# Kernel tuning notes

Measured on AMD Instinct MI355X. Metric: run time of the kernel, lower is better.

## Reference

```python
import jax, jax.numpy as jnp
import numpy as np

B, N, D_IN, D_OUT, NHOP = 16, 1024, 128, 128, 3


def setup_inputs() -> dict:
    key = jax.random.key(0)
    ks = jax.random.split(key, 7)
    x = jax.random.normal(ks[0], (B, N, D_IN), dtype=jnp.float32)
    # sparse-ish binary adjacency (float, as in the torch model) with self loops
    adj = (jax.random.uniform(ks[1], (B, N, N)) < 0.05).astype(jnp.float32)
    adj = jnp.maximum(adj, jnp.eye(N, dtype=jnp.float32)[None])
    # learned params (torch nn.Linear default-ish init scale)
    s_in = 1.0 / np.sqrt(D_IN)
    s_out = 1.0 / np.sqrt(2 * D_OUT)
    W_w = jax.random.uniform(ks[2], (D_OUT, D_IN), minval=-s_in, maxval=s_in, dtype=jnp.float32)
    W_b = jax.random.uniform(ks[3], (D_OUT,), minval=-s_in, maxval=s_in, dtype=jnp.float32)
    A = jax.random.normal(ks[4], (D_OUT, D_OUT), dtype=jnp.float32) * 0.02  # nn.Parameter(zeros) would kill signal; use small init
    gate_w = jax.random.uniform(ks[5], (1, 2 * D_OUT), minval=-s_out, maxval=s_out, dtype=jnp.float32)
    gate_b = jax.random.uniform(ks[6], (1,), minval=-s_out, maxval=s_out, dtype=jnp.float32)
    return {"x": x, "adj": adj, "W_w": W_w, "W_b": W_b, "A": A,
            "gate_w": gate_w, "gate_b": gate_b}


def reference(x, adj, W_w, W_b, A, gate_w, gate_b):
    # h = W(x): [B,N,D_OUT]
    h = jnp.einsum('bnd,od->bno', x, W_w) + W_b
    # bilinear score e[b,j,k] = (h A)_j . h_k, symmetrized
    e = jnp.einsum('bjl,bkl->bjk', jnp.einsum('bjd,de->bje', h, A), h)
    e = e + jnp.swapaxes(e, 1, 2)
    # masked softmax over dim=1 (as in the torch code), then re-mask
    att = jnp.where(adj > 0, e, jnp.zeros((), dtype=e.dtype))
    att = jax.nn.softmax(att, axis=1)
    att = att * adj
    retval = h
    for _ in range(NHOP):
        az = jax.nn.relu(jnp.einsum('bij,bjk->bik', att, retval))
        gate_in = jnp.concatenate([h, az], axis=-1)            # [B,N,2*D_OUT]
        coeff = jax.nn.sigmoid(jnp.einsum('bnf,of->bno', gate_in, gate_w) + gate_b)  # [B,N,1]
        retval = coeff * h + (1.0 - coeff) * az
    return retval
```

## Files before the change

kernel.cpp:

```cpp
#include <hip/hip_runtime.h>
#include <math.h>

#define Bn 16
#define Nn 1024
#define Dn 128

typedef unsigned short ushort;
typedef unsigned long long u64;
typedef short short8 __attribute__((ext_vector_type(8)));
typedef float f32x4 __attribute__((ext_vector_type(4)));
typedef ushort us8 __attribute__((ext_vector_type(8)));
typedef ushort us4 __attribute__((ext_vector_type(4)));

__device__ __forceinline__ ushort f2bf(float f) {
    unsigned u = __float_as_uint(f);
    u += 0x7fff + ((u >> 16) & 1);
    return (ushort)(u >> 16);
}
__device__ __forceinline__ float bf2f(ushort s) {
    return __uint_as_float(((unsigned)s) << 16);
}

#if defined(__has_builtin)
#if __has_builtin(__builtin_amdgcn_global_load_lds)
#define HAVE_GLL 1
#endif
#endif
#ifndef HAVE_GLL
#define HAVE_GLL 0
#endif

typedef __attribute__((address_space(1))) void as1_t;
typedef __attribute__((address_space(3))) void as3_t;

__device__ __forceinline__ void stage_group(const void* gbase, void* lbase, int lane) {
#if HAVE_GLL
    __builtin_amdgcn_global_load_lds((as1_t*)((const char*)gbase + lane * 16),
                                     (as3_t*)lbase, 16, 0, 0);
#else
    *(us8*)((char*)lbase + lane * 16) = *(const us8*)((const char*)gbase + lane * 16);
#endif
}


__global__ __launch_bounds__(256) void k_ph0(const float* __restrict__ Ww,
                                             const float* __restrict__ A,
                                             const float* __restrict__ adj,
                                             ushort* __restrict__ Whi, ushort* __restrict__ Wlo,
                                             ushort* __restrict__ Shi, ushort* __restrict__ Slo,
                                             float* __restrict__ Z, u64* __restrict__ bm) {
    int L = blockIdx.x, t = threadIdx.x;
    if (L < 64) {
        int i = L * 256 + t;
        float w = Ww[i];
        ushort wh = f2bf(w);
        Whi[i] = wh;
        Wlo[i] = f2bf(w - bf2f(wh));
        int e = i >> 7, d = i & 127;
        float s = A[i] + A[d * Dn + e];
        ushort sh = f2bf(s);
        Shi[i] = sh;
        Slo[i] = f2bf(s - bf2f(sh));
        Z[i] = (float)Nn;
    }
    int gwv = L * 4 + (t >> 6);
    int lane = t & 63;
    #pragma unroll 4
    for (int it = 0; it < 16; ++it) {
        int pair = gwv * 16 + it;
        const float* p = adj + (size_t)pair * 256 + lane * 4;
        float4 v = *(const float4*)p;
        u64 b0 = __ballot(v.x > 0.f);
        u64 b1 = __ballot(v.y > 0.f);
        u64 b2 = __ballot(v.z > 0.f);
        u64 b3 = __ballot(v.w > 0.f);
        if (lane == 0) {
            u64* d = bm + (size_t)pair * 4;
            d[0] = b0; d[1] = b1; d[2] = b2; d[3] = b3;
        }
    }
}

__global__ __launch_bounds__(256) void k_h(const float* __restrict__ x,
                                           const float* __restrict__ Wb,
                                           const ushort* __restrict__ Whi,
                                           const ushort* __restrict__ Wlo,
                                           const ushort* __restrict__ Shi,
                                           const ushort* __restrict__ Slo,
                                           float* __restrict__ h,
                                           ushort* __restrict__ h16f,
                                           ushort* __restrict__ g16f) {
    int I0 = blockIdx.x * 16;
    int t = threadIdx.x, w = t >> 6, lane = t & 63;
    int m = lane & 15, q = lane >> 4;

    __shared__ float xs[16][Dn + 4];
    __shared__ float hs[16][Dn + 4];
    __shared__ float gs_[16][Dn + 4];

    {
        int r = t >> 4, c8 = (t & 15) * 8;
        const float* src = x + (size_t)(I0 + r) * Dn + c8;
        *(float4*)&xs[r][c8]     = *(const float4*)(src);
        *(float4*)&xs[r][c8 + 4] = *(const float4*)(src + 4);
    }
    __syncthreads();

    f32x4 acc0 = {0,0,0,0}, acc1 = {0,0,0,0};
    #pragma unroll
    for (int ks = 0; ks < 4; ++ks) {
        int k0 = q * 8 + ks * 32;
        float v[8]; short8 ahi, alo;
        *(float4*)(v)     = *(const float4*)(&xs[m][k0]);
        *(float4*)(v + 4) = *(const float4*)(&xs[m][k0 + 4]);
        #pragma unroll
        for (int j = 0; j < 8; ++j) {
            ushort hi = f2bf(v[j]);
            ahi[j] = (short)hi;
            alo[j] = (short)f2bf(v[j] - bf2f(hi));
        }
        #pragma unroll
        for (int nn = 0; nn < 2; ++nn) {
            int brow = (w * 2 + nn) * 16 + m;
            short8 bhi = __builtin_bit_cast(short8, ((const us8*)(Whi + (size_t)brow * Dn))[q + ks * 4]);
            short8 blo = __builtin_bit_cast(short8, ((const us8*)(Wlo + (size_t)brow * Dn))[q + ks * 4]);
            f32x4 acc = nn ? acc1 : acc0;
            acc = __builtin_amdgcn_mfma_f32_16x16x32_bf16(ahi, bhi, acc, 0, 0, 0);
            acc = __builtin_amdgcn_mfma_f32_16x16x32_bf16(alo, bhi, acc, 0, 0, 0);
            acc = __builtin_amdgcn_mfma_f32_16x16x32_bf16(ahi, blo, acc, 0, 0, 0);
            if (nn) acc1 = acc; else acc0 = acc;
        }
    }
    #pragma unroll
    for (int nn = 0; nn < 2; ++nn) {
        int col = (w * 2 + nn) * 16 + m;
        float bias = Wb[col];
        f32x4 acc = nn ? acc1 : acc0;
        #pragma unroll
        for (int r = 0; r < 4; ++r) {
            int rl = q * 4 + r;
            float hv = acc[r] + bias;
            h[(size_t)(I0 + rl) * Dn + col] = hv;
            hs[rl][col] = hv;
        }
    }
    __syncthreads();

    f32x4 bcc0 = {0,0,0,0}, bcc1 = {0,0,0,0};
    #pragma unroll
    for (int ks = 0; ks < 4; ++ks) {
        int k0 = q * 8 + ks * 32;
        float v[8]; short8 ahi, alo;
        *(float4*)(v)     = *(const float4*)(&hs[m][k0]);
        *(float4*)(v + 4) = *(const float4*)(&hs[m][k0 + 4]);
        #pragma unroll
        for (int j = 0; j < 8; ++j) {
            ushort hi = f2bf(v[j]);
            ahi[j] = (short)hi;
            alo[j] = (short)f2bf(v[j] - bf2f(hi));
        }
        #pragma unroll
        for (int nn = 0; nn < 2; ++nn) {
            int brow = (w * 2 + nn) * 16 + m;
            short8 bhi = __builtin_bit_cast(short8, ((const us8*)(Shi + (size_t)brow * Dn))[q + ks * 4]);
            short8 blo = __builtin_bit_cast(short8, ((const us8*)(Slo + (size_t)brow * Dn))[q + ks * 4]);
            f32x4 acc = nn ? bcc1 : bcc0;
            acc = __builtin_amdgcn_mfma_f32_16x16x32_bf16(ahi, bhi, acc, 0, 0, 0);
            acc = __builtin_amdgcn_mfma_f32_16x16x32_bf16(alo, bhi, acc, 0, 0, 0);
            acc = __builtin_amdgcn_mfma_f32_16x16x32_bf16(ahi, blo, acc, 0, 0, 0);
            if (nn) bcc1 = acc; else bcc0 = acc;
        }
    }
    #pragma unroll
    for (int nn = 0; nn < 2; ++nn) {
        int col = (w * 2 + nn) * 16 + m;
        f32x4 acc = nn ? bcc1 : bcc0;
        #pragma unroll
        for (int r = 0; r < 4; ++r)
            gs_[q * 4 + r][col] = acc[r];
    }
    __syncthreads();

    {
        int kc = t >> 6, mm = (t >> 2) & 15, qq = t & 3;
        int cb = kc * 32 + qq * 8;
        us8 oh, oa;
        #pragma unroll
        for (int e = 0; e < 8; ++e) {
            oh[e] = f2bf(hs[mm][cb + e]);
            oa[e] = f2bf(gs_[mm][cb + e]);
        }
        size_t U = (size_t)(I0 >> 4) * 256 + kc * 64 + qq * 16 + mm;
        ((us8*)h16f)[U] = oh;
        ((us8*)g16f)[U] = oa;
    }
}

__global__ __launch_bounds__(256, 4) void k_scores(const ushort* __restrict__ g16f,
                                                   const ushort* __restrict__ h16f,
                                                   const u64* __restrict__ bm,
                                                   ushort* __restrict__ Ef,
                                                   float* __restrict__ Z) {
    int L = blockIdx.x;
    int b    = ((L & 7) << 1) | (L >> 11);
    int tile = (L >> 3) & 255;
    int I0 = (tile >> 4) << 6;
    int J0 = (tile & 15) << 6;
    int t = threadIdx.x, wid = t >> 6, lane = t & 63;
    int loff = lane * 16;

    __shared__ __align__(16) char smem[18432];
    float (*sc)[68] = (float(*)[68])smem;
    float (*cz)[64] = (float(*)[64])(smem + 17408);

    {
        const char* hbp = (const char*)h16f + (size_t)b * 262144;
        for (int g = wid; g < 16; g += 4) {
            int rt_l = g >> 2, kk = g & 3;
            stage_group(hbp + ((size_t)((J0 >> 4) + rt_l) * 256 + kk * 64) * 16,
                        smem + g * 1024, lane);
        }
    }
    short8 afr[4];
    {
        const char* gbp = (const char*)g16f + (size_t)b * 262144
                        + (size_t)((I0 >> 4) + wid) * 4096 + loff;
        #pragma unroll
        for (int ks = 0; ks < 4; ++ks)
            afr[ks] = __builtin_bit_cast(short8, *(const us8*)(gbp + ks * 1024));
    }
    __syncthreads();

    f32x4 acc[4] = {};
    #pragma unroll
    for (int ks = 0; ks < 4; ++ks) {
        #pragma unroll
        for (int nt = 0; nt < 4; ++nt) {
            short8 bb = __builtin_bit_cast(short8,
                *(const us8*)(smem + (nt * 4 + ks) * 1024 + loff));
            acc[nt] = __builtin_amdgcn_mfma_f32_16x16x32_bf16(afr[ks], bb, acc[nt], 0, 0, 0);
        }
    }
    __syncthreads();

    {
        int m = lane & 15, q = lane >> 4;
        #pragma unroll
        for (int nt = 0; nt < 4; ++nt)
            #pragma unroll
            for (int r = 0; r < 4; ++r)
                sc[wid * 16 + q * 4 + r][nt * 16 + m] = acc[nt][r];
    }
    __syncthreads();

    int row16 = t >> 4, c = t & 15;
    int bitc = ((J0 >> 2) & 63) + c;
    float colsum[4] = {0.f, 0.f, 0.f, 0.f};
    #pragma unroll
    for (int it = 0; it < 4; ++it) {
        int row = it * 16 + row16;
        const u64* wp = bm + ((size_t)(b * Nn + I0 + row) * 4 + (J0 >> 8)) * 4;
        u64 wj[4] = {wp[0], wp[1], wp[2], wp[3]};
        float s4[4];
        *(float4*)s4 = *(const float4*)(&sc[row][c * 4]);
        us4 e4;
        #pragma unroll
        for (int j = 0; j < 4; ++j) {
            float ex = __expf(s4[j]);
            bool on = (wj[j] >> bitc) & 1;
            e4[j] = f2bf(on ? ex : 0.f);
            colsum[j] += on ? (ex - 1.0f) : 0.f;
        }
        size_t base = ((((size_t)b * 64 + (I0 >> 4) + it) * 32 + (J0 >> 5) + (c >> 3)) * 512)
                    + (size_t)((c & 7) >> 1) * 128 + row16 * 8 + (c & 1) * 4;
        *(us4*)(Ef + base) = e4;
    }
    #pragma unroll
    for (int j = 0; j < 4; ++j) {
        colsum[j] += __shfl_xor(colsum[j], 16, 64);
        colsum[j] += __shfl_xor(colsum[j], 32, 64);
    }
    if (lane < 16) {
        #pragma unroll
        for (int j = 0; j < 4; ++j) cz[wid][lane * 4 + j] = colsum[j];
    }
    __syncthreads();
    if (t < 64) {
        float s = cz[0][t] + cz[1][t] + cz[2][t] + cz[3][t];
        atomicAdd(&Z[b * Nn + J0 + t], s);
    }
}

__global__ __launch_bounds__(256) void k_prep(const float* __restrict__ src,
                                              const float* __restrict__ Z,
                                              ushort* __restrict__ Tf) {
    int b = blockIdx.y;
    int j0 = blockIdx.x * 64;
    int t = threadIdx.x;
    __shared__ float ls[64][129];
    __shared__ float iz[64];
    if (t < 64) iz[t] = 1.0f / Z[b * Nn + j0 + t];
    __syncthreads();
    #pragma unroll
    for (int it = 0; it < 8; ++it) {
        int idx = it * 256 + t;
        int j = idx >> 5, k4 = (idx & 31) * 4;
        float4 v = *(const float4*)(src + ((size_t)b * Nn + j0 + j) * Dn + k4);
        float z = iz[j];
        ls[j][k4] = v.x * z; ls[j][k4 + 1] = v.y * z;
        ls[j][k4 + 2] = v.z * z; ls[j][k4 + 3] = v.w * z;
    }
    __syncthreads();
    int k = t & 127, half = t >> 7;
    us8 o[4];
    #pragma unroll
    for (int qq = 0; qq < 4; ++qq) {
        us8 tmp;
        #pragma unroll
        for (int e = 0; e < 8; ++e)
            tmp[e] = f2bf(ls[half * 32 + qq * 8 + e][k]);
        o[qq] = tmp;
    }
    size_t G = (size_t)(k >> 4) * 32 + (j0 >> 5) + half;
    ushort* dst = Tf + (size_t)b * 131072 + G * 512 + (size_t)(k & 15) * 8;
    #pragma unroll
    for (int qq = 0; qq < 4; ++qq)
        *(us8*)(dst + qq * 128) = o[qq];
}

#define STAGEB(BUF, cch) do {                                                          \
    for (int g = w; g < 32; g += 8)                                                    \
        stage_group(tfb + ((size_t)(g >> 2) * 32 + (cch) * 4 + (g & 3)) * 1024,        \
                    smem + (BUF) * 32768 + g * 1024, lane);                            \
} while (0)

#define ELOAD(SET, cch) do {                                                           \
    _Pragma("unroll")                                                                  \
    for (int kk = 0; kk < 4; ++kk)                                                     \
        SET[kk] = __builtin_bit_cast(short8,                                           \
            *(const us8*)(ebase + ((cch) * 4 + kk) * 1024));                           \
} while (0)

#define MFMAC(BUF, SET) do {                                                           \
    _Pragma("unroll")                                                                  \
    for (int kk = 0; kk < 4; ++kk) {                                                   \
        _Pragma("unroll")                                                              \
        for (int nt2 = 0; nt2 < 4; ++nt2) {                                            \
            short8 bf = __builtin_bit_cast(short8,                                     \
                *(const us8*)(smem + (BUF) * 32768 + choff + (nt2 * 4 + kk) * 1024 + loff)); \
            acc[nt2] = __builtin_amdgcn_mfma_f32_16x16x32_bf16(SET[kk], bf, acc[nt2], 0, 0, 0); \
        }                                                                              \
    }                                                                                  \
} while (0)

#define WAITB(NC) do {                                                                 \
    asm volatile("s_waitcnt vmcnt(" #NC ")" ::: "memory");                             \
    __builtin_amdgcn_s_barrier();                                                      \
} while (0)

__global__ __launch_bounds__(512, 1) void k_hop(const ushort* __restrict__ Ef,
                                                const ushort* __restrict__ Tf,
                                                const float* __restrict__ h,
                                                const float* __restrict__ Z,
                                                const float* __restrict__ gw,
                                                const float* __restrict__ gb,
                                                ushort* __restrict__ Tfn,
                                                float* __restrict__ out,
                                                int last) {
    int L = blockIdx.x;
    int b  = ((L & 7) << 1) | (L >> 7);
    int t4 = (L >> 3) & 15;
    int t = threadIdx.x, w = t >> 6, lane = t & 63;
    int m = lane & 15, q = lane >> 4;
    int wr = w & 3, ch = w >> 2;
    int rt = t4 * 4 + wr;
    int I0 = rt << 4;
    int loff = lane * 16;
    int choff = ch * 16384;

    __shared__ __align__(16) char smem[98304];
    __shared__ float gpart[4][16][2];

    const char* tfb   = (const char*)Tf + (size_t)b * 262144;
    const char* ebase = (const char*)Ef + (size_t)(b * 64 + rt) * 32768 + loff;

    f32x4 acc[4] = {};
    short8 aA[4], aB[4], aC[4];

    STAGEB(0, 0); ELOAD(aA, 0);
    STAGEB(1, 1); ELOAD(aB, 1);

    WAITB(8); STAGEB(2, 2); ELOAD(aC, 2); MFMAC(0, aA);
    WAITB(8); STAGEB(0, 3); ELOAD(aA, 3); MFMAC(1, aB);
    WAITB(8); STAGEB(1, 4); ELOAD(aB, 4); MFMAC(2, aC);
    WAITB(8); STAGEB(2, 5); ELOAD(aC, 5); MFMAC(0, aA);
    WAITB(8); STAGEB(0, 6); ELOAD(aA, 6); MFMAC(1, aB);
    WAITB(8); STAGEB(1, 7); ELOAD(aB, 7); MFMAC(2, aC);
    WAITB(8);                             MFMAC(0, aA);
    WAITB(0);                             MFMAC(1, aB);

    float gb0 = gb[0];
    float gwa[4], gwz[4];
    #pragma unroll
    for (int nt2 = 0; nt2 < 4; ++nt2) {
        gwa[nt2] = gw[ch * 64 + nt2 * 16 + m];
        gwz[nt2] = gw[Dn + ch * 64 + nt2 * 16 + m];
    }

    float hv[4][4], gsr[4];
    size_t hbase = ((size_t)b * Nn + I0) * Dn;
    #pragma unroll
    for (int r = 0; r < 4; ++r) {
        int row = q * 4 + r;
        float gs = 0.f;
        #pragma unroll
        for (int nt2 = 0; nt2 < 4; ++nt2) {
            float az = fmaxf(acc[nt2][r], 0.f);
            acc[nt2][r] = az;
            float hh = h[hbase + (size_t)row * Dn + ch * 64 + nt2 * 16 + m];
            hv[nt2][r] = hh;
            gs += hh * gwa[nt2] + az * gwz[nt2];
        }
        gs += __shfl_xor(gs, 1, 64);
        gs += __shfl_xor(gs, 2, 64);
        gs += __shfl_xor(gs, 4, 64);
        gs += __shfl_xor(gs, 8, 64);
        gsr[r] = gs;
    }
    if (m == 0) {
        #pragma unroll
        for (int r = 0; r < 4; ++r) gpart[wr][q * 4 + r][ch] = gsr[r];
    }
    __syncthreads();

    float coef[4];
    #pragma unroll
    for (int r = 0; r < 4; ++r) {
        float g2 = gpart[wr][q * 4 + r][0] + gpart[wr][q * 4 + r][1];
        coef[r] = 1.0f / (1.0f + __expf(-(g2 + gb0)));
    }

    if (last) {
        #pragma unroll
        for (int r = 0; r < 4; ++r) {
            int row = q * 4 + r;
            float cc = coef[r];
            #pragma unroll
            for (int nt2 = 0; nt2 < 4; ++nt2)
                out[hbase + (size_t)row * Dn + ch * 64 + nt2 * 16 + m] =
                    cc * hv[nt2][r] + (1.f - cc) * acc[nt2][r];
        }
    } else {
        ushort (*tt)[128][16] = (ushort(*)[128][16])smem;
        #pragma unroll
        for (int r = 0; r < 4; ++r) {
            int row = q * 4 + r;
            float cc = coef[r];
            float iz = 1.0f / Z[b * Nn + I0 + row];
            #pragma unroll
            for (int nt2 = 0; nt2 < 4; ++nt2) {
                float v = cc * hv[nt2][r] + (1.f - cc) * acc[nt2][r];
                tt[wr][ch * 64 + nt2 * 16 + m][row] = f2bf(v * iz);
            }
        }
        __syncthreads();
        if (t < 256) {
            int k = t >> 1, jh = t & 1;
            size_t G = (size_t)(k >> 4) * 32 + t4 * 2 + jh;
            ushort* dst = Tfn + (size_t)b * 131072 + G * 512 + (size_t)(k & 15) * 8;
            #pragma unroll
            for (int qq = 0; qq < 4; ++qq)
                *(us8*)(dst + qq * 128) = *(const us8*)&tt[jh * 2 + (qq >> 1)][k][(qq & 1) * 8];
        }
    }
}

extern "C" void kernel_launch(void* const* d_in, const int* in_sizes, int n_in,
                              void* d_out, int out_size, void* d_ws, size_t ws_size,
                              hipStream_t stream) {
    const float* x    = (const float*)d_in[0];
    const float* adj  = (const float*)d_in[1];
    const float* Ww   = (const float*)d_in[2];
    const float* Wb   = (const float*)d_in[3];
    const float* A    = (const float*)d_in[4];
    const float* gw   = (const float*)d_in[5];
    const float* gb   = (const float*)d_in[6];
    float* out = (float*)d_out;

    char* ws = (char*)d_ws;
    float*  h    = (float*)(ws);
    ushort* Ta   = (ushort*)(ws + (8u << 20));
    ushort* Tb   = (ushort*)(ws + (12u << 20));
    ushort* E    = (ushort*)(ws + (16u << 20));
    float*  Z    = (float*)(ws + (48u << 20));
    ushort* Whi  = (ushort*)(ws + (48u << 20) + (64u << 10));
    ushort* Wlo  = (ushort*)(ws + (48u << 20) + (96u << 10));
    ushort* Shi  = (ushort*)(ws + (48u << 20) + (128u << 10));
    ushort* Slo  = (ushort*)(ws + (48u << 20) + (160u << 10));
    u64*    bm   = (u64*)(ws + (48u << 20) + (192u << 10));

    k_ph0   <<<1024, 256, 0, stream>>>(Ww, A, adj, Whi, Wlo, Shi, Slo, Z, bm);
    k_h     <<<1024, 256, 0, stream>>>(x, Wb, Whi, Wlo, Shi, Slo, h, Ta, Tb);
    k_scores<<<4096, 256, 0, stream>>>(Tb, Ta, bm, E, Z);
    k_prep  <<<dim3(16, Bn), 256, 0, stream>>>(h, Z, Ta);
    k_hop   <<<256, 512, 0, stream>>>(E, Ta, h, Z, gw, gb, Tb, out, 0);
    k_hop   <<<256, 512, 0, stream>>>(E, Tb, h, Z, gw, gb, Ta, out, 0);
    k_hop   <<<256, 512, 0, stream>>>(E, Ta, h, Z, gw, gb, (ushort*)nullptr, out, 1);
}
```

Baseline: 192.1 us.

## Fuse hop kernels into one persistent kernel with grid barriers; fold prep and bitmask

Replaces the prep kernel and the three separate hop launches with a single persistent kernel of 128 blocks. Each block handles two row tiles and uses an atomic-counter grid barrier between hops, and it keeps h and 1/Z in registers across hops. The adjacency bitmask build moves into k_h, and the k_scores epilogue is rewritten to write 8-wide E stores with shuffle-based column sums. This removes launch overhead and repeated h loads, but halves the grid size, which cuts parallelism per hop, and adds spin-barrier costs that assume all blocks are co-resident.

```diff
diff --git a/kernel.cpp b/kernel.cpp
--- a/kernel.cpp
+++ b/kernel.cpp
@@ -42,29 +42,158 @@
 #endif
 }
 
-
-__global__ __launch_bounds__(256) void k_ph0(const float* __restrict__ Ww,
-                                             const float* __restrict__ A,
-                                             const float* __restrict__ adj,
-                                             ushort* __restrict__ Whi, ushort* __restrict__ Wlo,
-                                             ushort* __restrict__ Shi, ushort* __restrict__ Slo,
-                                             float* __restrict__ Z, u64* __restrict__ bm) {
-    int L = blockIdx.x, t = threadIdx.x;
-    if (L < 64) {
-        int i = L * 256 + t;
-        float w = Ww[i];
-        ushort wh = f2bf(w);
-        Whi[i] = wh;
-        Wlo[i] = f2bf(w - bf2f(wh));
-        int e = i >> 7, d = i & 127;
-        float s = A[i] + A[d * Dn + e];
-        ushort sh = f2bf(s);
-        Shi[i] = sh;
-        Slo[i] = f2bf(s - bf2f(sh));
-        Z[i] = (float)Nn;
-    }
-    int gwv = L * 4 + (t >> 6);
-    int lane = t & 63;
+__device__ __forceinline__ void gbar(int* bar, int phase, int nblk) {
+    __syncthreads();
+    if (threadIdx.x == 0) {
+        __threadfence();
+        int old = atomicAdd(&bar[0], 1);
+        if (old == phase * nblk - 1)
+            __hip_atomic_store(&bar[1], phase, __ATOMIC_RELAXED, __HIP_MEMORY_SCOPE_AGENT);
+        while (__hip_atomic_load(&bar[1], __ATOMIC_RELAXED, __HIP_MEMORY_SCOPE_AGENT) < phase)
+            __builtin_amdgcn_s_sleep(2);
+        __threadfence();
+    }
+    __syncthreads();
+}
+
+
+__global__ __launch_bounds__(256) void k_W(const float* __restrict__ Ww,
+                                           const float* __restrict__ A,
+                                           ushort* __restrict__ Whi, ushort* __restrict__ Wlo,
+                                           ushort* __restrict__ Shi, ushort* __restrict__ Slo,
+                                           float* __restrict__ Z, int* __restrict__ bar) {
+    int i = blockIdx.x * 256 + threadIdx.x;
+    float w = Ww[i];
+    ushort wh = f2bf(w);
+    Whi[i] = wh;
+    Wlo[i] = f2bf(w - bf2f(wh));
+    int e = i >> 7, d = i & 127;
+    float s = A[i] + A[d * Dn + e];
+    ushort sh = f2bf(s);
+    Shi[i] = sh;
+    Slo[i] = f2bf(s - bf2f(sh));
+    Z[i] = (float)Nn;
+    if (i == 0) { bar[0] = 0; bar[1] = 0; }
+}
+
+__global__ __launch_bounds__(256) void k_h(const float* __restrict__ x,
+                                           const float* __restrict__ adj,
+                                           const float* __restrict__ Wb,
+                                           const ushort* __restrict__ Whi,
+                                           const ushort* __restrict__ Wlo,
+                                           const ushort* __restrict__ Shi,
+                                           const ushort* __restrict__ Slo,
+                                           float* __restrict__ h,
+                                           ushort* __restrict__ h16f,
+                                           ushort* __restrict__ g16f,
+                                           u64* __restrict__ bm) {
+    int L = blockIdx.x;
+    int I0 = L * 16;
+    int t = threadIdx.x, w = t >> 6, lane = t & 63;
+    int m = lane & 15, q = lane >> 4;
+
+    __shared__ float xs[16][Dn + 4];
+    __shared__ float hs[16][Dn + 4];
+    __shared__ float gs_[16][Dn + 4];
+
+    {
+        int r = t >> 4, c8 = (t & 15) * 8;
+        const float* src = x + (size_t)(I0 + r) * Dn + c8;
+        *(float4*)&xs[r][c8]     = *(const float4*)(src);
+        *(float4*)&xs[r][c8 + 4] = *(const float4*)(src + 4);
+    }
+    __syncthreads();
+
+    f32x4 acc0 = {0,0,0,0}, acc1 = {0,0,0,0};
+    #pragma unroll
+    for (int ks = 0; ks < 4; ++ks) {
+        int k0 = q * 8 + ks * 32;
+        float v[8]; short8 ahi, alo;
+        *(float4*)(v)     = *(const float4*)(&xs[m][k0]);
+        *(float4*)(v + 4) = *(const float4*)(&xs[m][k0 + 4]);
+        #pragma unroll
+        for (int j = 0; j < 8; ++j) {
+            ushort hi = f2bf(v[j]);
+            ahi[j] = (short)hi;
+            alo[j] = (short)f2bf(v[j] - bf2f(hi));
+        }
+        #pragma unroll
+        for (int nn = 0; nn < 2; ++nn) {
+            int brow = (w * 2 + nn) * 16 + m;
+            short8 bhi = __builtin_bit_cast(short8, ((const us8*)(Whi + (size_t)brow * Dn))[q + ks * 4]);
+            short8 blo = __builtin_bit_cast(short8, ((const us8*)(Wlo + (size_t)brow * Dn))[q + ks * 4]);
+            f32x4 acc = nn ? acc1 : acc0;
+            acc = __builtin_amdgcn_mfma_f32_16x16x32_bf16(ahi, bhi, acc, 0, 0, 0);
+            acc = __builtin_amdgcn_mfma_f32_16x16x32_bf16(alo, bhi, acc, 0, 0, 0);
+            acc = __builtin_amdgcn_mfma_f32_16x16x32_bf16(ahi, blo, acc, 0, 0, 0);
+            if (nn) acc1 = acc; else acc0 = acc;
+        }
+    }
+    #pragma unroll
+    for (int nn = 0; nn < 2; ++nn) {
+        int col = (w * 2 + nn) * 16 + m;
+        float bias = Wb[col];
+        f32x4 acc = nn ? acc1 : acc0;
+        #pragma unroll
+        for (int r = 0; r < 4; ++r) {
+            int rl = q * 4 + r;
+            float hv = acc[r] + bias;
+            h[(size_t)(I0 + rl) * Dn + col] = hv;
+            hs[rl][col] = hv;
+        }
+    }
+    __syncthreads();
+
+    f32x4 bcc0 = {0,0,0,0}, bcc1 = {0,0,0,0};
+    #pragma unroll
+    for (int ks = 0; ks < 4; ++ks) {
+        int k0 = q * 8 + ks * 32;
+        float v[8]; short8 ahi, alo;
+        *(float4*)(v)     = *(const float4*)(&hs[m][k0]);
+        *(float4*)(v + 4) = *(const float4*)(&hs[m][k0 + 4]);
+        #pragma unroll
+        for (int j = 0; j < 8; ++j) {
+            ushort hi = f2bf(v[j]);
+            ahi[j] = (short)hi;
+            alo[j] = (short)f2bf(v[j] - bf2f(hi));
+        }
+        #pragma unroll
+        for (int nn = 0; nn < 2; ++nn) {
+            int brow = (w * 2 + nn) * 16 + m;
+            short8 bhi = __builtin_bit_cast(short8, ((const us8*)(Shi + (size_t)brow * Dn))[q + ks * 4]);
+            short8 blo = __builtin_bit_cast(short8, ((const us8*)(Slo + (size_t)brow * Dn))[q + ks * 4]);
+            f32x4 acc = nn ? bcc1 : bcc0;
+            acc = __builtin_amdgcn_mfma_f32_16x16x32_bf16(ahi, bhi, acc, 0, 0, 0);
+            acc = __builtin_amdgcn_mfma_f32_16x16x32_bf16(alo, bhi, acc, 0, 0, 0);
+            acc = __builtin_amdgcn_mfma_f32_16x16x32_bf16(ahi, blo, acc, 0, 0, 0);
+            if (nn) bcc1 = acc; else bcc0 = acc;
+        }
+    }
+    #pragma unroll
+    for (int nn = 0; nn < 2; ++nn) {
+        int col = (w * 2 + nn) * 16 + m;
+        f32x4 acc = nn ? bcc1 : bcc0;
+        #pragma unroll
+        for (int r = 0; r < 4; ++r)
+            gs_[q * 4 + r][col] = acc[r];
+    }
+    __syncthreads();
+
+    {
+        int kc = t >> 6, mm = (t >> 2) & 15, qq = t & 3;
+        int cb = kc * 32 + qq * 8;
+        us8 oh, oa;
+        #pragma unroll
+        for (int e = 0; e < 8; ++e) {
+            oh[e] = f2bf(hs[mm][cb + e]);
+            oa[e] = f2bf(gs_[mm][cb + e]);
+        }
+        size_t U = (size_t)L * 256 + kc * 64 + qq * 16 + mm;
+        ((us8*)h16f)[U] = oh;
+        ((us8*)g16f)[U] = oa;
+    }
+
+    int gwv = L * 4 + w;
     #pragma unroll 4
     for (int it = 0; it < 16; ++it) {
         int pair = gwv * 16 + it;
@@ -81,121 +210,6 @@
     }
 }
 
-__global__ __launch_bounds__(256) void k_h(const float* __restrict__ x,
-                                           const float* __restrict__ Wb,
-                                           const ushort* __restrict__ Whi,
-                                           const ushort* __restrict__ Wlo,
-                                           const ushort* __restrict__ Shi,
-                                           const ushort* __restrict__ Slo,
-                                           float* __restrict__ h,
-                                           ushort* __restrict__ h16f,
-                                           ushort* __restrict__ g16f) {
-    int I0 = blockIdx.x * 16;
-    int t = threadIdx.x, w = t >> 6, lane = t & 63;
-    int m = lane & 15, q = lane >> 4;
-
-    __shared__ float xs[16][Dn + 4];
-    __shared__ float hs[16][Dn + 4];
-    __shared__ float gs_[16][Dn + 4];
-
-    {
-        int r = t >> 4, c8 = (t & 15) * 8;
-        const float* src = x + (size_t)(I0 + r) * Dn + c8;
-        *(float4*)&xs[r][c8]     = *(const float4*)(src);
-        *(float4*)&xs[r][c8 + 4] = *(const float4*)(src + 4);
-    }
-    __syncthreads();
-
-    f32x4 acc0 = {0,0,0,0}, acc1 = {0,0,0,0};
-    #pragma unroll
-    for (int ks = 0; ks < 4; ++ks) {
-        int k0 = q * 8 + ks * 32;
-        float v[8]; short8 ahi, alo;
-        *(float4*)(v)     = *(const float4*)(&xs[m][k0]);
-        *(float4*)(v + 4) = *(const float4*)(&xs[m][k0 + 4]);
-        #pragma unroll
-        for (int j = 0; j < 8; ++j) {
-            ushort hi = f2bf(v[j]);
-            ahi[j] = (short)hi;
-            alo[j] = (short)f2bf(v[j] - bf2f(hi));
-        }
-        #pragma unroll
-        for (int nn = 0; nn < 2; ++nn) {
-            int brow = (w * 2 + nn) * 16 + m;
-            short8 bhi = __builtin_bit_cast(short8, ((const us8*)(Whi + (size_t)brow * Dn))[q + ks * 4]);
-            short8 blo = __builtin_bit_cast(short8, ((const us8*)(Wlo + (size_t)brow * Dn))[q + ks * 4]);
-            f32x4 acc = nn ? acc1 : acc0;
-            acc = __builtin_amdgcn_mfma_f32_16x16x32_bf16(ahi, bhi, acc, 0, 0, 0);
-            acc = __builtin_amdgcn_mfma_f32_16x16x32_bf16(alo, bhi, acc, 0, 0, 0);
-            acc = __builtin_amdgcn_mfma_f32_16x16x32_bf16(ahi, blo, acc, 0, 0, 0);
-            if (nn) acc1 = acc; else acc0 = acc;
-        }
-    }
-    #pragma unroll
-    for (int nn = 0; nn < 2; ++nn) {
-        int col = (w * 2 + nn) * 16 + m;
-        float bias = Wb[col];
-        f32x4 acc = nn ? acc1 : acc0;
-        #pragma unroll
-        for (int r = 0; r < 4; ++r) {
-            int rl = q * 4 + r;
-            float hv = acc[r] + bias;
-            h[(size_t)(I0 + rl) * Dn + col] = hv;
-            hs[rl][col] = hv;
-        }
-    }
-    __syncthreads();
-
-    f32x4 bcc0 = {0,0,0,0}, bcc1 = {0,0,0,0};
-    #pragma unroll
-    for (int ks = 0; ks < 4; ++ks) {
-        int k0 = q * 8 + ks * 32;
-        float v[8]; short8 ahi, alo;
-        *(float4*)(v)     = *(const float4*)(&hs[m][k0]);
-        *(float4*)(v + 4) = *(const float4*)(&hs[m][k0 + 4]);
-        #pragma unroll
-        for (int j = 0; j < 8; ++j) {
-            ushort hi = f2bf(v[j]);
-            ahi[j] = (short)hi;
-            alo[j] = (short)f2bf(v[j] - bf2f(hi));
-        }
-        #pragma unroll
-        for (int nn = 0; nn < 2; ++nn) {
-            int brow = (w * 2 + nn) * 16 + m;
-            short8 bhi = __builtin_bit_cast(short8, ((const us8*)(Shi + (size_t)brow * Dn))[q + ks * 4]);
-            short8 blo = __builtin_bit_cast(short8, ((const us8*)(Slo + (size_t)brow * Dn))[q + ks * 4]);
-            f32x4 acc = nn ? bcc1 : bcc0;
-            acc = __builtin_amdgcn_mfma_f32_16x16x32_bf16(ahi, bhi, acc, 0, 0, 0);
-            acc = __builtin_amdgcn_mfma_f32_16x16x32_bf16(alo, bhi, acc, 0, 0, 0);
-            acc = __builtin_amdgcn_mfma_f32_16x16x32_bf16(ahi, blo, acc, 0, 0, 0);
-            if (nn) bcc1 = acc; else bcc0 = acc;
-        }
-    }
-    #pragma unroll
-    for (int nn = 0; nn < 2; ++nn) {
-        int col = (w * 2 + nn) * 16 + m;
-        f32x4 acc = nn ? bcc1 : bcc0;
-        #pragma unroll
-        for (int r = 0; r < 4; ++r)
-            gs_[q * 4 + r][col] = acc[r];
-    }
-    __syncthreads();
-
-    {
-        int kc = t >> 6, mm = (t >> 2) & 15, qq = t & 3;
-        int cb = kc * 32 + qq * 8;
-        us8 oh, oa;
-        #pragma unroll
-        for (int e = 0; e < 8; ++e) {
-            oh[e] = f2bf(hs[mm][cb + e]);
-            oa[e] = f2bf(gs_[mm][cb + e]);
-        }
-        size_t U = (size_t)(I0 >> 4) * 256 + kc * 64 + qq * 16 + mm;
-        ((us8*)h16f)[U] = oh;
-        ((us8*)g16f)[U] = oa;
-    }
-}
-
 __global__ __launch_bounds__(256, 4) void k_scores(const ushort* __restrict__ g16f,
                                                    const ushort* __restrict__ h16f,
                                                    const u64* __restrict__ bm,
@@ -211,7 +225,7 @@
 
     __shared__ __align__(16) char smem[18432];
     float (*sc)[68] = (float(*)[68])smem;
-    float (*cz)[64] = (float(*)[64])(smem + 17408);
+    float (*cz8)[32] = (float(*)[32])(smem + 17408);
 
     {
         const char* hbp = (const char*)h16f + (size_t)b * 262144;
@@ -253,79 +267,44 @@
     }
     __syncthreads();
 
-    int row16 = t >> 4, c = t & 15;
-    int bitc = ((J0 >> 2) & 63) + c;
-    float colsum[4] = {0.f, 0.f, 0.f, 0.f};
-    #pragma unroll
-    for (int it = 0; it < 4; ++it) {
-        int row = it * 16 + row16;
+    int mm = lane & 15, qq = lane >> 4;
+    #pragma unroll
+    for (int rep = 0; rep < 2; ++rep) {
+        int gidx = wid + rep * 4;
+        int it = gidx >> 1, kcg = gidx & 1;
+        int row = it * 16 + mm;
+        int c0 = kcg * 32 + qq * 8;
         const u64* wp = bm + ((size_t)(b * Nn + I0 + row) * 4 + (J0 >> 8)) * 4;
         u64 wj[4] = {wp[0], wp[1], wp[2], wp[3]};
-        float s4[4];
-        *(float4*)s4 = *(const float4*)(&sc[row][c * 4]);
-        us4 e4;
-        #pragma unroll
-        for (int j = 0; j < 4; ++j) {
-            float ex = __expf(s4[j]);
-            bool on = (wj[j] >> bitc) & 1;
-            e4[j] = f2bf(on ? ex : 0.f);
-            colsum[j] += on ? (ex - 1.0f) : 0.f;
-        }
-        size_t base = ((((size_t)b * 64 + (I0 >> 4) + it) * 32 + (J0 >> 5) + (c >> 3)) * 512)
-                    + (size_t)((c & 7) >> 1) * 128 + row16 * 8 + (c & 1) * 4;
-        *(us4*)(Ef + base) = e4;
-    }
-    #pragma unroll
-    for (int j = 0; j < 4; ++j) {
-        colsum[j] += __shfl_xor(colsum[j], 16, 64);
-        colsum[j] += __shfl_xor(colsum[j], 32, 64);
-    }
-    if (lane < 16) {
-        #pragma unroll
-        for (int j = 0; j < 4; ++j) cz[wid][lane * 4 + j] = colsum[j];
+        int bitbase = ((J0 + c0) >> 2) & 63;
+        float s8[8];
+        *(float4*)(s8)     = *(const float4*)(&sc[row][c0]);
+        *(float4*)(s8 + 4) = *(const float4*)(&sc[row][c0 + 4]);
+        us8 e8; float cs[8];
+        #pragma unroll
+        for (int e = 0; e < 8; ++e) {
+            float ex = __expf(s8[e]);
+            bool on = (wj[e & 3] >> (bitbase + (e >> 2))) & 1;
+            e8[e] = f2bf(on ? ex : 0.f);
+            cs[e] = on ? ex - 1.0f : 0.f;
+        }
+        size_t G = ((size_t)b * 64 + (I0 >> 4) + it) * 32 + (J0 >> 5) + kcg;
+        *(us8*)(Ef + G * 512 + (size_t)lane * 8) = e8;
+        #pragma unroll
+        for (int msk = 1; msk <= 8; msk <<= 1)
+            #pragma unroll
+            for (int e = 0; e < 8; ++e) cs[e] += __shfl_xor(cs[e], msk, 64);
+        if (mm == 0) {
+            #pragma unroll
+            for (int e = 0; e < 8; ++e) cz8[gidx][qq * 8 + e] = cs[e];
+        }
     }
     __syncthreads();
     if (t < 64) {
-        float s = cz[0][t] + cz[1][t] + cz[2][t] + cz[3][t];
-        atomicAdd(&Z[b * Nn + J0 + t], s);
-    }
-}
-
-__global__ __launch_bounds__(256) void k_prep(const float* __restrict__ src,
-                                              const float* __restrict__ Z,
-                                              ushort* __restrict__ Tf) {
-    int b = blockIdx.y;
-    int j0 = blockIdx.x * 64;
-    int t = threadIdx.x;
-    __shared__ float ls[64][129];
-    __shared__ float iz[64];
-    if (t < 64) iz[t] = 1.0f / Z[b * Nn + j0 + t];
-    __syncthreads();
-    #pragma unroll
-    for (int it = 0; it < 8; ++it) {
-        int idx = it * 256 + t;
-        int j = idx >> 5, k4 = (idx & 31) * 4;
-        float4 v = *(const float4*)(src + ((size_t)b * Nn + j0 + j) * Dn + k4);
-        float z = iz[j];
-        ls[j][k4] = v.x * z; ls[j][k4 + 1] = v.y * z;
-        ls[j][k4 + 2] = v.z * z; ls[j][k4 + 3] = v.w * z;
-    }
-    __syncthreads();
-    int k = t & 127, half = t >> 7;
-    us8 o[4];
-    #pragma unroll
-    for (int qq = 0; qq < 4; ++qq) {
-        us8 tmp;
-        #pragma unroll
-        for (int e = 0; e < 8; ++e)
-            tmp[e] = f2bf(ls[half * 32 + qq * 8 + e][k]);
-        o[qq] = tmp;
-    }
-    size_t G = (size_t)(k >> 4) * 32 + (j0 >> 5) + half;
-    ushort* dst = Tf + (size_t)b * 131072 + G * 512 + (size_t)(k & 15) * 8;
-    #pragma unroll
-    for (int qq = 0; qq < 4; ++qq)
-        *(us8*)(dst + qq * 128) = o[qq];
+        int kcg = t >> 5, cc = t & 31;
+        float s = cz8[kcg][cc] + cz8[2 + kcg][cc] + cz8[4 + kcg][cc] + cz8[6 + kcg][cc];
+        atomicAdd(&Z[b * Nn + J0 + kcg * 32 + cc], s);
+    }
 }
 
 #define STAGEB(BUF, cch) do {                                                          \
@@ -358,46 +337,27 @@
     __builtin_amdgcn_s_barrier();                                                      \
 } while (0)
 
-__global__ __launch_bounds__(512, 1) void k_hop(const ushort* __restrict__ Ef,
-                                                const ushort* __restrict__ Tf,
-                                                const float* __restrict__ h,
-                                                const float* __restrict__ Z,
-                                                const float* __restrict__ gw,
-                                                const float* __restrict__ gb,
-                                                ushort* __restrict__ Tfn,
-                                                float* __restrict__ out,
-                                                int last) {
+__global__ __launch_bounds__(512, 1) void k_hops(const ushort* __restrict__ Ef,
+                                                 const float* __restrict__ h,
+                                                 const float* __restrict__ Z,
+                                                 const float* __restrict__ gw,
+                                                 const float* __restrict__ gb,
+                                                 ushort* __restrict__ T0,
+                                                 ushort* __restrict__ T1,
+                                                 float* __restrict__ out,
+                                                 int* __restrict__ bar) {
     int L = blockIdx.x;
-    int b  = ((L & 7) << 1) | (L >> 7);
-    int t4 = (L >> 3) & 15;
+    int xcd = L & 7, sub = L >> 3;
+    int b = xcd * 2 + (sub >> 3);
+    int tp = sub & 7;
     int t = threadIdx.x, w = t >> 6, lane = t & 63;
     int m = lane & 15, q = lane >> 4;
     int wr = w & 3, ch = w >> 2;
-    int rt = t4 * 4 + wr;
-    int I0 = rt << 4;
     int loff = lane * 16;
     int choff = ch * 16384;
 
     __shared__ __align__(16) char smem[98304];
     __shared__ float gpart[4][16][2];
-
-    const char* tfb   = (const char*)Tf + (size_t)b * 262144;
-    const char* ebase = (const char*)Ef + (size_t)(b * 64 + rt) * 32768 + loff;
-
-    f32x4 acc[4] = {};
-    short8 aA[4], aB[4], aC[4];
-
-    STAGEB(0, 0); ELOAD(aA, 0);
-    STAGEB(1, 1); ELOAD(aB, 1);
-
-    WAITB(8); STAGEB(2, 2); ELOAD(aC, 2); MFMAC(0, aA);
-    WAITB(8); STAGEB(0, 3); ELOAD(aA, 3); MFMAC(1, aB);
-    WAITB(8); STAGEB(1, 4); ELOAD(aB, 4); MFMAC(2, aC);
-    WAITB(8); STAGEB(2, 5); ELOAD(aC, 5); MFMAC(0, aA);
-    WAITB(8); STAGEB(0, 6); ELOAD(aA, 6); MFMAC(1, aB);
-    WAITB(8); STAGEB(1, 7); ELOAD(aB, 7); MFMAC(2, aC);
-    WAITB(8);                             MFMAC(0, aA);
-    WAITB(0);                             MFMAC(1, aB);
 
     float gb0 = gb[0];
     float gwa[4], gwz[4];
@@ -407,71 +367,130 @@
         gwz[nt2] = gw[Dn + ch * 64 + nt2 * 16 + m];
     }
 
-    float hv[4][4], gsr[4];
-    size_t hbase = ((size_t)b * Nn + I0) * Dn;
-    #pragma unroll
-    for (int r = 0; r < 4; ++r) {
-        int row = q * 4 + r;
-        float gs = 0.f;
-        #pragma unroll
-        for (int nt2 = 0; nt2 < 4; ++nt2) {
-            float az = fmaxf(acc[nt2][r], 0.f);
-            acc[nt2][r] = az;
-            float hh = h[hbase + (size_t)row * Dn + ch * 64 + nt2 * 16 + m];
-            hv[nt2][r] = hh;
-            gs += hh * gwa[nt2] + az * gwz[nt2];
-        }
-        gs += __shfl_xor(gs, 1, 64);
-        gs += __shfl_xor(gs, 2, 64);
-        gs += __shfl_xor(gs, 4, 64);
-        gs += __shfl_xor(gs, 8, 64);
-        gsr[r] = gs;
-    }
-    if (m == 0) {
-        #pragma unroll
-        for (int r = 0; r < 4; ++r) gpart[wr][q * 4 + r][ch] = gsr[r];
-    }
-    __syncthreads();
-
-    float coef[4];
-    #pragma unroll
-    for (int r = 0; r < 4; ++r) {
-        float g2 = gpart[wr][q * 4 + r][0] + gpart[wr][q * 4 + r][1];
-        coef[r] = 1.0f / (1.0f + __expf(-(g2 + gb0)));
-    }
-
-    if (last) {
+    float hv[2][4][4], izr[2][4];
+
+    #pragma unroll
+    for (int tile = 0; tile < 2; ++tile) {
+        int t4v = tp * 2 + tile;
+        int rt = t4v * 4 + wr;
+        int I0 = rt << 4;
+        size_t hbase = ((size_t)b * Nn + I0) * Dn;
         #pragma unroll
         for (int r = 0; r < 4; ++r) {
             int row = q * 4 + r;
-            float cc = coef[r];
+            izr[tile][r] = 1.0f / Z[b * Nn + I0 + row];
             #pragma unroll
             for (int nt2 = 0; nt2 < 4; ++nt2)
-                out[hbase + (size_t)row * Dn + ch * 64 + nt2 * 16 + m] =
-                    cc * hv[nt2][r] + (1.f - cc) * acc[nt2][r];
-        }
-    } else {
+                hv[tile][nt2][r] = h[hbase + (size_t)row * Dn + ch * 64 + nt2 * 16 + m];
+        }
         ushort (*tt)[128][16] = (ushort(*)[128][16])smem;
         #pragma unroll
-        for (int r = 0; r < 4; ++r) {
-            int row = q * 4 + r;
-            float cc = coef[r];
-            float iz = 1.0f / Z[b * Nn + I0 + row];
-            #pragma unroll
-            for (int nt2 = 0; nt2 < 4; ++nt2) {
-                float v = cc * hv[nt2][r] + (1.f - cc) * acc[nt2][r];
-                tt[wr][ch * 64 + nt2 * 16 + m][row] = f2bf(v * iz);
-            }
-        }
+        for (int r = 0; r < 4; ++r)
+            #pragma unroll
+            for (int nt2 = 0; nt2 < 4; ++nt2)
+                tt[wr][ch * 64 + nt2 * 16 + m][q * 4 + r] = f2bf(hv[tile][nt2][r] * izr[tile][r]);
         __syncthreads();
         if (t < 256) {
             int k = t >> 1, jh = t & 1;
-            size_t G = (size_t)(k >> 4) * 32 + t4 * 2 + jh;
-            ushort* dst = Tfn + (size_t)b * 131072 + G * 512 + (size_t)(k & 15) * 8;
+            size_t G = (size_t)(k >> 4) * 32 + t4v * 2 + jh;
+            ushort* dst = T0 + (size_t)b * 131072 + G * 512 + (size_t)(k & 15) * 8;
             #pragma unroll
             for (int qq = 0; qq < 4; ++qq)
                 *(us8*)(dst + qq * 128) = *(const us8*)&tt[jh * 2 + (qq >> 1)][k][(qq & 1) * 8];
         }
+        __syncthreads();
+    }
+    gbar(bar, 1, 128);
+
+    #pragma unroll 1
+    for (int hop = 0; hop < 3; ++hop) {
+        const char* tfb = (const char*)(hop == 1 ? T1 : T0) + (size_t)b * 262144;
+        ushort* Tout = (hop == 0) ? T1 : T0;
+        #pragma unroll
+        for (int tile = 0; tile < 2; ++tile) {
+            int t4v = tp * 2 + tile;
+            int rt = t4v * 4 + wr;
+            int I0 = rt << 4;
+            const char* ebase = (const char*)Ef + (size_t)(b * 64 + rt) * 32768 + loff;
+
+            f32x4 acc[4] = {};
+            short8 aA[4], aB[4], aC[4];
+            STAGEB(0, 0); ELOAD(aA, 0);
+            STAGEB(1, 1); ELOAD(aB, 1);
+            WAITB(8); STAGEB(2, 2); ELOAD(aC, 2); MFMAC(0, aA);
+            WAITB(8); STAGEB(0, 3); ELOAD(aA, 3); MFMAC(1, aB);
+            WAITB(8); STAGEB(1, 4); ELOAD(aB, 4); MFMAC(2, aC);
+            WAITB(8); STAGEB(2, 5); ELOAD(aC, 5); MFMAC(0, aA);
+            WAITB(8); STAGEB(0, 6); ELOAD(aA, 6); MFMAC(1, aB);
+            WAITB(8); STAGEB(1, 7); ELOAD(aB, 7); MFMAC(2, aC);
+            WAITB(8);                             MFMAC(0, aA);
+            WAITB(0);                             MFMAC(1, aB);
+
+            float gsr[4];
+            #pragma unroll
+            for (int r = 0; r < 4; ++r) {
+                float gs = 0.f;
+                #pragma unroll
+                for (int nt2 = 0; nt2 < 4; ++nt2) {
+                    float az = fmaxf(acc[nt2][r], 0.f);
+                    acc[nt2][r] = az;
+                    gs += hv[tile][nt2][r] * gwa[nt2] + az * gwz[nt2];
+                }
+                gs += __shfl_xor(gs, 1, 64);
+                gs += __shfl_xor(gs, 2, 64);
+                gs += __shfl_xor(gs, 4, 64);
+                gs += __shfl_xor(gs, 8, 64);
+                gsr[r] = gs;
+            }
+            if (m == 0) {
+                #pragma unroll
+                for (int r = 0; r < 4; ++r) gpart[wr][q * 4 + r][ch] = gsr[r];
+            }
+            __syncthreads();
+
+            float coef[4];
+            #pragma unroll
+            for (int r = 0; r < 4; ++r) {
+                float g2 = gpart[wr][q * 4 + r][0] + gpart[wr][q * 4 + r][1];
+                coef[r] = 1.0f / (1.0f + __expf(-(g2 + gb0)));
+            }
+
+            if (hop == 2) {
+                size_t hbase = ((size_t)b * Nn + I0) * Dn;
+                #pragma unroll
+                for (int r = 0; r < 4; ++r) {
+                    int row = q * 4 + r;
+                    float cc = coef[r];
+                    #pragma unroll
+                    for (int nt2 = 0; nt2 < 4; ++nt2)
+                        out[hbase + (size_t)row * Dn + ch * 64 + nt2 * 16 + m] =
+                            cc * hv[tile][nt2][r] + (1.f - cc) * acc[nt2][r];
+                }
+            } else {
+                ushort (*tt)[128][16] = (ushort(*)[128][16])smem;
+                #pragma unroll
+                for (int r = 0; r < 4; ++r) {
+                    float cc = coef[r];
+                    float iz = izr[tile][r];
+                    #pragma unroll
+                    for (int nt2 = 0; nt2 < 4; ++nt2) {
+                        float v = cc * hv[tile][nt2][r] + (1.f - cc) * acc[nt2][r];
+                        tt[wr][ch * 64 + nt2 * 16 + m][q * 4 + r] = f2bf(v * iz);
+                    }
+                }
+                __syncthreads();
+                if (t < 256) {
+                    int k = t >> 1, jh = t & 1;
+                    size_t G = (size_t)(k >> 4) * 32 + t4v * 2 + jh;
+                    ushort* dst = Tout + (size_t)b * 131072 + G * 512 + (size_t)(k & 15) * 8;
+                    #pragma unroll
+                    for (int qq = 0; qq < 4; ++qq)
+                        *(us8*)(dst + qq * 128) = *(const us8*)&tt[jh * 2 + (qq >> 1)][k][(qq & 1) * 8];
+                }
+                __syncthreads();
+            }
+        }
+        if (hop < 2) gbar(bar, 2 + hop, 128);
     }
 }
 
@@ -498,12 +517,10 @@
     ushort* Shi  = (ushort*)(ws + (48u << 20) + (128u << 10));
     ushort* Slo  = (ushort*)(ws + (48u << 20) + (160u << 10));
     u64*    bm   = (u64*)(ws + (48u << 20) + (192u << 10));
-
-    k_ph0   <<<1024, 256, 0, stream>>>(Ww, A, adj, Whi, Wlo, Shi, Slo, Z, bm);
-    k_h     <<<1024, 256, 0, stream>>>(x, Wb, Whi, Wlo, Shi, Slo, h, Ta, Tb);
+    int*    bar  = (int*)(ws + (51u << 20));
+
+    k_W     <<<64,   256, 0, stream>>>(Ww, A, Whi, Wlo, Shi, Slo, Z, bar);
+    k_h     <<<1024, 256, 0, stream>>>(x, adj, Wb, Whi, Wlo, Shi, Slo, h, Ta, Tb, bm);
     k_scores<<<4096, 256, 0, stream>>>(Tb, Ta, bm, E, Z);
-    k_prep  <<<dim3(16, Bn), 256, 0, stream>>>(h, Z, Ta);
-    k_hop   <<<256, 512, 0, stream>>>(E, Ta, h, Z, gw, gb, Tb, out, 0);
-    k_hop   <<<256, 512, 0, stream>>>(E, Tb, h, Z, gw, gb, Ta, out, 0);
-    k_hop   <<<256, 512, 0, stream>>>(E, Ta, h, Z, gw, gb, (ushort*)nullptr, out, 1);
-}
+    k_hops  <<<128,  512, 0, stream>>>(E, h, Z, gw, gb, Ta, Tb, out, bar);
+}
```

Measured after the change: 272.3 us. 41.7% more time.

## Drop LDS staging in hop kernel; read B fragments directly from global

Applied to the files above, without the earlier changes.

Rewrites the hop kernel from 512-thread blocks with a triple-buffered LDS pipeline (global_load_lds staging and barriers) into 256-thread blocks that load MFMA B operands straight from global/L2 per lane. The grid doubles to 512 blocks and the barrier-synchronised staging is removed, aiming for more occupancy and less sync. In exchange, the T operand is no longer shared across waves through LDS, so global/L2 traffic rises, and the loop has no software prefetch to hide load latency. The 1/Z reciprocal is also hoisted before the main loop.

```diff
diff --git a/kernel.cpp b/kernel.cpp
--- a/kernel.cpp
+++ b/kernel.cpp
@@ -328,76 +328,55 @@
         *(us8*)(dst + qq * 128) = o[qq];
 }
 
-#define STAGEB(BUF, cch) do {                                                          \
-    for (int g = w; g < 32; g += 8)                                                    \
-        stage_group(tfb + ((size_t)(g >> 2) * 32 + (cch) * 4 + (g & 3)) * 1024,        \
-                    smem + (BUF) * 32768 + g * 1024, lane);                            \
-} while (0)
-
-#define ELOAD(SET, cch) do {                                                           \
-    _Pragma("unroll")                                                                  \
-    for (int kk = 0; kk < 4; ++kk)                                                     \
-        SET[kk] = __builtin_bit_cast(short8,                                           \
-            *(const us8*)(ebase + ((cch) * 4 + kk) * 1024));                           \
-} while (0)
-
-#define MFMAC(BUF, SET) do {                                                           \
-    _Pragma("unroll")                                                                  \
-    for (int kk = 0; kk < 4; ++kk) {                                                   \
-        _Pragma("unroll")                                                              \
-        for (int nt2 = 0; nt2 < 4; ++nt2) {                                            \
-            short8 bf = __builtin_bit_cast(short8,                                     \
-                *(const us8*)(smem + (BUF) * 32768 + choff + (nt2 * 4 + kk) * 1024 + loff)); \
-            acc[nt2] = __builtin_amdgcn_mfma_f32_16x16x32_bf16(SET[kk], bf, acc[nt2], 0, 0, 0); \
-        }                                                                              \
-    }                                                                                  \
-} while (0)
-
-#define WAITB(NC) do {                                                                 \
-    asm volatile("s_waitcnt vmcnt(" #NC ")" ::: "memory");                             \
-    __builtin_amdgcn_s_barrier();                                                      \
-} while (0)
-
-__global__ __launch_bounds__(512, 1) void k_hop(const ushort* __restrict__ Ef,
-                                                const ushort* __restrict__ Tf,
-                                                const float* __restrict__ h,
-                                                const float* __restrict__ Z,
-                                                const float* __restrict__ gw,
-                                                const float* __restrict__ gb,
-                                                ushort* __restrict__ Tfn,
-                                                float* __restrict__ out,
-                                                int last) {
+__global__ __launch_bounds__(256) void k_hop(const ushort* __restrict__ Ef,
+                                             const ushort* __restrict__ Tf,
+                                             const float* __restrict__ h,
+                                             const float* __restrict__ Z,
+                                             const float* __restrict__ gw,
+                                             const float* __restrict__ gb,
+                                             ushort* __restrict__ Tfn,
+                                             float* __restrict__ out,
+                                             int last) {
     int L = blockIdx.x;
-    int b  = ((L & 7) << 1) | (L >> 7);
-    int t4 = (L >> 3) & 15;
+    int b   = ((L & 7) << 1) | (L >> 8);
+    int rtp = (L >> 3) & 31;
     int t = threadIdx.x, w = t >> 6, lane = t & 63;
     int m = lane & 15, q = lane >> 4;
-    int wr = w & 3, ch = w >> 2;
-    int rt = t4 * 4 + wr;
+    int rr = w & 1, ch = w >> 1;
+    int rt = rtp * 2 + rr;
     int I0 = rt << 4;
     int loff = lane * 16;
-    int choff = ch * 16384;
-
-    __shared__ __align__(16) char smem[98304];
-    __shared__ float gpart[4][16][2];
-
-    const char* tfb   = (const char*)Tf + (size_t)b * 262144;
+
+    __shared__ ushort tt[2][128][16];
+    __shared__ float gpart[2][16][2];
+
     const char* ebase = (const char*)Ef + (size_t)(b * 64 + rt) * 32768 + loff;
+    const char* tb    = (const char*)Tf + (size_t)b * 262144 + (size_t)ch * 131072 + loff;
+
+    float izr[4];
+    #pragma unroll
+    for (int r = 0; r < 4; ++r)
+        izr[r] = 1.0f / Z[b * Nn + I0 + q * 4 + r];
 
     f32x4 acc[4] = {};
-    short8 aA[4], aB[4], aC[4];
-
-    STAGEB(0, 0); ELOAD(aA, 0);
-    STAGEB(1, 1); ELOAD(aB, 1);
-
-    WAITB(8); STAGEB(2, 2); ELOAD(aC, 2); MFMAC(0, aA);
-    WAITB(8); STAGEB(0, 3); ELOAD(aA, 3); MFMAC(1, aB);
-    WAITB(8); STAGEB(1, 4); ELOAD(aB, 4); MFMAC(2, aC);
-    WAITB(8); STAGEB(2, 5); ELOAD(aC, 5); MFMAC(0, aA);
-    WAITB(8); STAGEB(0, 6); ELOAD(aA, 6); MFMAC(1, aB);
-    WAITB(8); STAGEB(1, 7); ELOAD(aB, 7); MFMAC(2, aC);
-    WAITB(8);                             MFMAC(0, aA);
-    WAITB(0);                             MFMAC(1, aB);
+    #pragma unroll 1
+    for (int cch = 0; cch < 8; ++cch) {
+        const char* eb = ebase + (size_t)cch * 4096;
+        const char* tc = tb + (size_t)cch * 4096;
+        short8 ea[4];
+        #pragma unroll
+        for (int kk = 0; kk < 4; ++kk)
+            ea[kk] = __builtin_bit_cast(short8, *(const us8*)(eb + kk * 1024));
+        #pragma unroll
+        for (int kk = 0; kk < 4; ++kk) {
+            #pragma unroll
+            for (int nt2 = 0; nt2 < 4; ++nt2) {
+                short8 bf = __builtin_bit_cast(short8,
+                    *(const us8*)(tc + (size_t)nt2 * 32768 + kk * 1024));
+                acc[nt2] = __builtin_amdgcn_mfma_f32_16x16x32_bf16(ea[kk], bf, acc[nt2], 0, 0, 0);
+            }
+        }
+    }
 
     float gb0 = gb[0];
     float gwa[4], gwz[4];
@@ -429,14 +408,14 @@
     }
     if (m == 0) {
         #pragma unroll
-        for (int r = 0; r < 4; ++r) gpart[wr][q * 4 + r][ch] = gsr[r];
+        for (int r = 0; r < 4; ++r) gpart[rr][q * 4 + r][ch] = gsr[r];
     }
     __syncthreads();
 
     float coef[4];
     #pragma unroll
     for (int r = 0; r < 4; ++r) {
-        float g2 = gpart[wr][q * 4 + r][0] + gpart[wr][q * 4 + r][1];
+        float g2 = gpart[rr][q * 4 + r][0] + gpart[rr][q * 4 + r][1];
         coef[r] = 1.0f / (1.0f + __expf(-(g2 + gb0)));
     }
 
@@ -451,26 +430,24 @@
                     cc * hv[nt2][r] + (1.f - cc) * acc[nt2][r];
         }
     } else {
-        ushort (*tt)[128][16] = (ushort(*)[128][16])smem;
         #pragma unroll
         for (int r = 0; r < 4; ++r) {
-            int row = q * 4 + r;
             float cc = coef[r];
-            float iz = 1.0f / Z[b * Nn + I0 + row];
+            float iz = izr[r];
             #pragma unroll
             for (int nt2 = 0; nt2 < 4; ++nt2) {
                 float v = cc * hv[nt2][r] + (1.f - cc) * acc[nt2][r];
-                tt[wr][ch * 64 + nt2 * 16 + m][row] = f2bf(v * iz);
+                tt[rr][ch * 64 + nt2 * 16 + m][q * 4 + r] = f2bf(v * iz);
             }
         }
         __syncthreads();
-        if (t < 256) {
-            int k = t >> 1, jh = t & 1;
-            size_t G = (size_t)(k >> 4) * 32 + t4 * 2 + jh;
-            ushort* dst = Tfn + (size_t)b * 131072 + G * 512 + (size_t)(k & 15) * 8;
-            #pragma unroll
-            for (int qq = 0; qq < 4; ++qq)
-                *(us8*)(dst + qq * 128) = *(const us8*)&tt[jh * 2 + (qq >> 1)][k][(qq & 1) * 8];
+        int k = t >> 1, jh = t & 1;
+        size_t Gb = (size_t)b * 131072 + ((size_t)(k >> 4) * 32 + rtp) * 512 + (size_t)(k & 15) * 8;
+        #pragma unroll
+        for (int u2 = 0; u2 < 2; ++u2) {
+            int qq = jh * 2 + u2;
+            *(us8*)(Tfn + Gb + (size_t)qq * 128) =
+                *(const us8*)&tt[qq >> 1][k][(qq & 1) * 8];
         }
     }
 }
@@ -503,7 +480,7 @@
     k_h     <<<1024, 256, 0, stream>>>(x, Wb, Whi, Wlo, Shi, Slo, h, Ta, Tb);
     k_scores<<<4096, 256, 0, stream>>>(Tb, Ta, bm, E, Z);
     k_prep  <<<dim3(16, Bn), 256, 0, stream>>>(h, Z, Ta);
-    k_hop   <<<256, 512, 0, stream>>>(E, Ta, h, Z, gw, gb, Tb, out, 0);
-    k_hop   <<<256, 512, 0, stream>>>(E, Tb, h, Z, gw, gb, Ta, out, 0);
-    k_hop   <<<256, 512, 0, stream>>>(E, Ta, h, Z, gw, gb, (ushort*)nullptr, out, 1);
-}
+    k_hop   <<<512, 256, 0, stream>>>(E, Ta, h, Z, gw, gb, Tb, out, 0);
+    k_hop   <<<512, 256, 0, stream>>>(E, Tb, h, Z, gw, gb, Ta, out, 0);
+    k_hop   <<<512, 256, 0, stream>>>(E, Ta, h, Z, gw, gb, (ushort*)nullptr, out, 1);
+}
```

After: 260.6 us. 35.7% more time.
